# Kernel tuning notes

Hardware: AMD Instinct MI355X
Metric: run time of the kernel (lower is better)

## Reference

```python
import jax, jax.numpy as jnp
import numpy as np

DIM = 1024
EPS_LN = 1e-5
EPS_MEM = 1e-6

def _layernorm(x, g, b):
    mu = jnp.mean(x, axis=-1, keepdims=True)
    var = jnp.mean((x - mu) ** 2, axis=-1, keepdims=True)
    return (x - mu) * jax.lax.rsqrt(var + EPS_LN) * g + b

def setup_inputs() -> dict:
    key = jax.random.key(0)
    ks = jax.random.split(key, 8)
    B, S, D = 4, 4096, DIM
    s1 = 1.0 / np.sqrt(D)
    s2 = 1.0 / np.sqrt(4 * D)
    return {
        "x": jax.random.normal(ks[0], (B, S, D), dtype=jnp.float32),
        "ln1_g": jnp.ones((D,), jnp.float32),
        "ln1_b": jnp.zeros((D,), jnp.float32),
        "ln2_g": jnp.ones((D,), jnp.float32),
        "ln2_b": jnp.zeros((D,), jnp.float32),
        "gate_w": jax.random.uniform(ks[1], (D, D), jnp.float32, -s1, s1),
        "gate_b": jax.random.uniform(ks[2], (D,), jnp.float32, -s1, s1),
        "value_w": jax.random.uniform(ks[3], (D, D), jnp.float32, -s1, s1),
        "value_b": jax.random.uniform(ks[4], (D,), jnp.float32, -s1, s1),
        "ffn_w1": jax.random.uniform(ks[5], (D, 4 * D), jnp.float32, -s1, s1),
        "ffn_b1": jnp.zeros((4 * D,), jnp.float32),
        "ffn_w2": jax.random.uniform(ks[6], (4 * D, D), jnp.float32, -s2, s2),
        "ffn_b2": jnp.zeros((D,), jnp.float32),
    }

def reference(x, ln1_g, ln1_b, ln2_g, ln2_b, gate_w, gate_b, value_w, value_b, ffn_w1, ffn_b1, ffn_w2, ffn_b2):
    h = _layernorm(x, ln1_g, ln1_b)
    g = jax.nn.sigmoid(h @ gate_w + gate_b)
    v = h @ value_w + value_b
    cumsum_v = jnp.cumsum(g * v, axis=1)
    cumsum_g = jnp.cumsum(g, axis=1) + EPS_MEM
    x = x + cumsum_v / cumsum_g
    h2 = _layernorm(x, ln2_g, ln2_b)
    ffn = jax.nn.gelu(h2 @ ffn_w1 + ffn_b1, approximate=False) @ ffn_w2 + ffn_b2
    return x + ffn
```

## Files before the change

### kernel.cpp

```cpp
#include <hip/hip_runtime.h>
#include <cstdint>
#include <cstddef>

#define D_MODEL 1024
#define SEQ     4096
#define BATCH   4
#define M_ROWS  (BATCH*SEQ)
#define NCHUNK  64
#define LCHUNK  (SEQ/NCHUNK)

typedef __bf16 bf16_t;
typedef __bf16 bf16x8 __attribute__((ext_vector_type(8)));
typedef __bf16 bf16x4 __attribute__((ext_vector_type(4)));
typedef float  f32x4  __attribute__((ext_vector_type(4)));

__device__ __forceinline__ void load_lds_128(const bf16_t* g, bf16_t* l) {
    __builtin_amdgcn_global_load_lds(
        (const __attribute__((address_space(1))) unsigned int*)g,
        (__attribute__((address_space(3))) unsigned int*)l,
        16, 0, 0);
}

__device__ __forceinline__ float2 bf16pair_to_f2(unsigned int u) {
    union { unsigned int i; float f; } a, b;
    a.i = u << 16;
    b.i = u & 0xffff0000u;
    float2 r; r.x = a.f; r.y = b.f; return r;
}

__global__ __launch_bounds__(256)
void transpose_all(const float* __restrict__ gate_w, const float* __restrict__ value_w,
                   const float* __restrict__ ffn_w1, const float* __restrict__ ffn_w2,
                   bf16_t* __restrict__ wgv_t, bf16_t* __restrict__ w1_t,
                   bf16_t* __restrict__ w2_t) {
    int id = blockIdx.x;
    const float* in; bf16_t* outp; int R, C, bx, by;
    if (id < 1024)      { in = gate_w;  outp = wgv_t;               R = 1024; C = 1024; bx = id & 31;  by = id >> 5; }
    else if (id < 2048) { id -= 1024; in = value_w; outp = wgv_t + 1024*1024; R = 1024; C = 1024; bx = id & 31;  by = id >> 5; }
    else if (id < 6144) { id -= 2048; in = ffn_w1;  outp = w1_t;    R = 1024; C = 4096; bx = id & 127; by = id >> 7; }
    else                { id -= 6144; in = ffn_w2;  outp = w2_t;    R = 4096; C = 1024; bx = id & 31;  by = id >> 5; }
    __shared__ float t[32][33];
    int tx = threadIdx.x & 31, ty = threadIdx.x >> 5;
    int c0 = bx * 32, r0 = by * 32;
    #pragma unroll
    for (int j = 0; j < 32; j += 8)
        t[ty + j][tx] = in[(size_t)(r0 + ty + j) * C + c0 + tx];
    __syncthreads();
    #pragma unroll
    for (int j = 0; j < 32; j += 8)
        outp[(size_t)(c0 + ty + j) * R + r0 + tx] = (bf16_t)t[tx][ty + j];
}

__global__ __launch_bounds__(256)
void ln_kernel(const float* __restrict__ x, const float* __restrict__ gamma,
               const float* __restrict__ beta, bf16_t* __restrict__ h) {
    int row = blockIdx.x;
    int tid = threadIdx.x;
    const float4* xr = (const float4*)(x + (size_t)row * D_MODEL);
    float4 v = xr[tid];
    float s  = v.x + v.y + v.z + v.w;
    float ss = v.x*v.x + v.y*v.y + v.z*v.z + v.w*v.w;
    #pragma unroll
    for (int off = 32; off; off >>= 1) {
        s  += __shfl_down(s, off);
        ss += __shfl_down(ss, off);
    }
    __shared__ float red[8];
    int wave = tid >> 6, lane = tid & 63;
    if (lane == 0) { red[wave] = s; red[4 + wave] = ss; }
    __syncthreads();
    if (tid == 0) {
        float S  = red[0] + red[1] + red[2] + red[3];
        float SS = red[4] + red[5] + red[6] + red[7];
        float mean = S * (1.0f / D_MODEL);
        float var  = SS * (1.0f / D_MODEL) - mean * mean;
        red[0] = mean;
        red[1] = rsqrtf(var + 1e-5f);
    }
    __syncthreads();
    float mean = red[0], rstd = red[1];
    float4 gv = ((const float4*)gamma)[tid];
    float4 bv = ((const float4*)beta)[tid];
    bf16x4 o;
    o[0] = (bf16_t)((v.x - mean) * rstd * gv.x + bv.x);
    o[1] = (bf16_t)((v.y - mean) * rstd * gv.y + bv.y);
    o[2] = (bf16_t)((v.z - mean) * rstd * gv.z + bv.z);
    o[3] = (bf16_t)((v.w - mean) * rstd * gv.w + bv.w);
    ((bf16x4*)h)[(size_t)row * (D_MODEL / 4) + tid] = o;
}

template <int MODE, int TN>
__global__ __launch_bounds__(256, 4)
void gemm_kernel(const bf16_t* __restrict__ A, const bf16_t* __restrict__ Bt,
                 const float* __restrict__ bias, const float* __restrict__ bias2,
                 const float* __restrict__ xres,
                 void* __restrict__ out, void* __restrict__ out2,
                 int M, int N, int K) {
    __shared__ __align__(16) bf16_t ldsA[128 * 64];
    __shared__ __align__(16) bf16_t ldsB[128 * 64];

    const int tid  = threadIdx.x;
    const int lane = tid & 63;
    const int wave = tid >> 6;
    const int wm   = wave & 1;
    const int wn   = wave >> 1;

    const int L  = blockIdx.x;
    const int r  = L >> 3;
    const int n0 = (r % TN) * 128;
    const int m0 = ((L & 7) + 8 * (r / TN)) * 128;

    f32x4 acc[4][4];
    f32x4 zero = {0.f, 0.f, 0.f, 0.f};
    #pragma unroll
    for (int i = 0; i < 4; i++)
        #pragma unroll
        for (int j = 0; j < 4; j++) acc[i][j] = zero;

    const int rl     = lane >> 3;
    const int srcCol = ((lane & 7) ^ rl) * 8;

    const int quad = lane >> 4;
    const int l16  = lane & 15;
    const int rswz = l16 & 7;

    for (int k0 = 0; k0 < K; k0 += 64) {
        __syncthreads();
        #pragma unroll
        for (int i = 0; i < 4; i++) {
            int cb = i * 4 + wave;
            int rr = cb * 8 + rl;
            load_lds_128(A  + (size_t)(m0 + rr) * K + k0 + srcCol,
                         ldsA + cb * 512 + lane * 8);
            load_lds_128(Bt + (size_t)(n0 + rr) * K + k0 + srcCol,
                         ldsB + cb * 512 + lane * 8);
        }
        __syncthreads();

        #pragma unroll
        for (int kk = 0; kk < 2; kk++) {
            int pos = ((quad + 4 * kk) ^ rswz) * 8;
            bf16x8 af[4], bfr[4];
            #pragma unroll
            for (int mt = 0; mt < 4; mt++)
                af[mt] = *(const bf16x8*)(ldsA + (wm * 64 + mt * 16 + l16) * 64 + pos);
            #pragma unroll
            for (int nt = 0; nt < 4; nt++)
                bfr[nt] = *(const bf16x8*)(ldsB + (wn * 64 + nt * 16 + l16) * 64 + pos);
            #pragma unroll
            for (int mt = 0; mt < 4; mt++)
                #pragma unroll
                for (int nt = 0; nt < 4; nt++)
                    acc[mt][nt] = __builtin_amdgcn_mfma_f32_16x16x32_bf16(
                        bfr[nt], af[mt], acc[mt][nt], 0, 0, 0);
        }
    }

    #pragma unroll
    for (int mt = 0; mt < 4; mt++) {
        int row = m0 + wm * 64 + mt * 16 + l16;
        #pragma unroll
        for (int nt = 0; nt < 4; nt++) {
            int col = n0 + wn * 64 + nt * 16 + quad * 4;
            f32x4 a = acc[mt][nt];
            if (MODE == 4) {
                bool isV = (n0 >= 1024);
                int c1 = col & 1023;
                float4 bv = *(const float4*)((isV ? bias2 : bias) + c1);
                float4 val;
                val.x = a[0] + bv.x; val.y = a[1] + bv.y;
                val.z = a[2] + bv.z; val.w = a[3] + bv.w;
                if (!isV) {
                    val.x = 1.0f / (1.0f + __expf(-val.x));
                    val.y = 1.0f / (1.0f + __expf(-val.y));
                    val.z = 1.0f / (1.0f + __expf(-val.z));
                    val.w = 1.0f / (1.0f + __expf(-val.w));
                }
                bf16x4 p;
                p[0] = (bf16_t)val.x; p[1] = (bf16_t)val.y;
                p[2] = (bf16_t)val.z; p[3] = (bf16_t)val.w;
                bf16_t* o = (bf16_t*)(isV ? out2 : out);
                *(bf16x4*)(o + (size_t)row * 1024 + c1) = p;
            } else if (MODE == 2) {
                float4 bv = *(const float4*)(bias + col);
                float4 val;
                val.x = a[0] + bv.x; val.y = a[1] + bv.y;
                val.z = a[2] + bv.z; val.w = a[3] + bv.w;
                val.x = 0.5f * val.x * (1.0f + erff(val.x * 0.70710678118654752f));
                val.y = 0.5f * val.y * (1.0f + erff(val.y * 0.70710678118654752f));
                val.z = 0.5f * val.z * (1.0f + erff(val.z * 0.70710678118654752f));
                val.w = 0.5f * val.w * (1.0f + erff(val.w * 0.70710678118654752f));
                bf16x4 p;
                p[0] = (bf16_t)val.x; p[1] = (bf16_t)val.y;
                p[2] = (bf16_t)val.z; p[3] = (bf16_t)val.w;
                *(bf16x4*)((bf16_t*)out + (size_t)row * N + col) = p;
            } else {
                float4 bv = *(const float4*)(bias + col);
                float4 xr = *(const float4*)(xres + (size_t)row * N + col);
                float4 val;
                val.x = xr.x + a[0] + bv.x; val.y = xr.y + a[1] + bv.y;
                val.z = xr.z + a[2] + bv.z; val.w = xr.w + a[3] + bv.w;
                *(float4*)((float*)out + (size_t)row * N + col) = val;
            }
        }
    }
}

__global__ __launch_bounds__(256)
void scan_partial(const bf16_t* __restrict__ g, const bf16_t* __restrict__ v,
                  float* __restrict__ sg, float* __restrict__ sgv) {
    int dt = blockIdx.x & 1;
    int c  = (blockIdx.x >> 1) & (NCHUNK - 1);
    int b  = blockIdx.x >> 7;
    int d  = dt * 512 + threadIdx.x * 2;
    float s0 = 0.f, s1 = 0.f, t0 = 0.f, t1 = 0.f;
    for (int i = 0; i < LCHUNK; i++) {
        int s = c * LCHUNK + i;
        size_t idx = ((size_t)(b * SEQ + s)) * D_MODEL + d;
        float2 gf = bf16pair_to_f2(*(const unsigned int*)(g + idx));
        float2 vf = bf16pair_to_f2(*(const unsigned int*)(v + idx));
        s0 += gf.x; s1 += gf.y;
        t0 += gf.x * vf.x; t1 += gf.y * vf.y;
    }
    size_t o = ((size_t)(b * NCHUNK + c)) * D_MODEL + d;
    sg[o] = s0;  sg[o + 1] = s1;
    sgv[o] = t0; sgv[o + 1] = t1;
}

__global__ __launch_bounds__(256)
void scan_apply(const bf16_t* __restrict__ g, const bf16_t* __restrict__ v,
                const float* __restrict__ x, const float* __restrict__ sg,
                const float* __restrict__ sgv, float* __restrict__ out) {
    int dt = blockIdx.x & 1;
    int c  = (blockIdx.x >> 1) & (NCHUNK - 1);
    int b  = blockIdx.x >> 7;
    int d  = dt * 512 + threadIdx.x * 2;
    float rg0 = 0.f, rg1 = 0.f, rv0 = 0.f, rv1 = 0.f;
    for (int p = 0; p < c; p++) {
        size_t o = ((size_t)(b * NCHUNK + p)) * D_MODEL + d;
        float2 a  = *(const float2*)(sg + o);
        float2 bb = *(const float2*)(sgv + o);
        rg0 += a.x;  rg1 += a.y;
        rv0 += bb.x; rv1 += bb.y;
    }
    for (int i = 0; i < LCHUNK; i++) {
        int s = c * LCHUNK + i;
        size_t idx = ((size_t)(b * SEQ + s)) * D_MODEL + d;
        float2 gf = bf16pair_to_f2(*(const unsigned int*)(g + idx));
        float2 vf = bf16pair_to_f2(*(const unsigned int*)(v + idx));
        rv0 += gf.x * vf.x; rg0 += gf.x;
        rv1 += gf.y * vf.y; rg1 += gf.y;
        float2 xv = *(const float2*)(x + idx);
        float2 ov;
        ov.x = xv.x + rv0 / (rg0 + 1e-6f);
        ov.y = xv.y + rv1 / (rg1 + 1e-6f);
        *(float2*)(out + idx) = ov;
    }
}

extern "C" void kernel_launch(void* const* d_in, const int* in_sizes, int n_in,
                              void* d_out, int out_size, void* d_ws, size_t ws_size,
                              hipStream_t stream) {
    (void)in_sizes; (void)n_in; (void)out_size; (void)ws_size;
    const float* x       = (const float*)d_in[0];
    const float* ln1_g   = (const float*)d_in[1];
    const float* ln1_b   = (const float*)d_in[2];
    const float* ln2_g   = (const float*)d_in[3];
    const float* ln2_b   = (const float*)d_in[4];
    const float* gate_w  = (const float*)d_in[5];
    const float* gate_b  = (const float*)d_in[6];
    const float* value_w = (const float*)d_in[7];
    const float* value_b = (const float*)d_in[8];
    const float* ffn_w1  = (const float*)d_in[9];
    const float* ffn_b1  = (const float*)d_in[10];
    const float* ffn_w2  = (const float*)d_in[11];
    const float* ffn_b2  = (const float*)d_in[12];
    float* out = (float*)d_out;

    char* ws = (char*)d_ws;
    const size_t MB = 1024 * 1024;
    bf16_t* wgv_t = (bf16_t*)(ws + 0 * MB);
    bf16_t* w1_t  = (bf16_t*)(ws + 4 * MB);
    bf16_t* w2_t  = (bf16_t*)(ws + 12 * MB);
    bf16_t* h     = (bf16_t*)(ws + 20 * MB);
    bf16_t* g     = (bf16_t*)(ws + 52 * MB);
    bf16_t* v     = (bf16_t*)(ws + 84 * MB);
    float*  sg    = (float*)(ws + 116 * MB);
    float*  sgv   = (float*)(ws + 117 * MB);
    bf16_t* act   = (bf16_t*)(ws + 118 * MB);

    transpose_all<<<10240, 256, 0, stream>>>(gate_w, value_w, ffn_w1, ffn_w2,
                                             wgv_t, w1_t, w2_t);

    ln_kernel<<<M_ROWS, 256, 0, stream>>>(x, ln1_g, ln1_b, h);

    gemm_kernel<4, 16><<<(2048 / 128) * (M_ROWS / 128), 256, 0, stream>>>(
        h, wgv_t, gate_b, value_b, nullptr, g, v, M_ROWS, 2048, 1024);

    scan_partial<<<BATCH * NCHUNK * 2, 256, 0, stream>>>(g, v, sg, sgv);
    scan_apply<<<BATCH * NCHUNK * 2, 256, 0, stream>>>(g, v, x, sg, sgv, out);

    ln_kernel<<<M_ROWS, 256, 0, stream>>>(out, ln2_g, ln2_b, h);

    gemm_kernel<2, 32><<<(4096 / 128) * (M_ROWS / 128), 256, 0, stream>>>(
        h, w1_t, ffn_b1, nullptr, nullptr, act, nullptr, M_ROWS, 4096, 1024);

    gemm_kernel<3, 8><<<(1024 / 128) * (M_ROWS / 128), 256, 0, stream>>>(
        act, w2_t, ffn_b2, nullptr, out, out, nullptr, M_ROWS, 1024, 4096);
}
```

Measured before the change: 637.3 us.

## Replace GEMM with 256x256 double-buffered 8-wave pipelined kernel

Replaces the 128x128 single-buffered GEMM with a 256x256 tile kernel using 512 threads, double-buffered LDS, and a phased schedule. The schedule interleaves global-to-LDS loads with MFMA groups, using barriers and s_setprio. The aim is to overlap memory traffic with compute and to raise reuse per loaded tile. In exchange it uses 128 KB of LDS and many accumulator registers per block, which limits occupancy to one block per CU and risks register pressure. All three GEMM launches are updated with the new grid sizes.

```diff
diff --git a/kernel.cpp b/kernel.cpp
--- a/kernel.cpp
+++ b/kernel.cpp
@@ -89,78 +89,126 @@
     ((bf16x4*)h)[(size_t)row * (D_MODEL / 4) + tid] = o;
 }
 
+#define PHASE_MID() do { __builtin_amdgcn_s_barrier(); \
+    asm volatile("s_waitcnt lgkmcnt(0)" ::: "memory"); \
+    __builtin_amdgcn_s_setprio(1); } while (0)
+#define PHASE_END() do { __builtin_amdgcn_s_setprio(0); \
+    __builtin_amdgcn_s_barrier(); } while (0)
+#define PHASE_END_VM() do { __builtin_amdgcn_s_setprio(0); \
+    asm volatile("s_waitcnt vmcnt(4)" ::: "memory"); \
+    __builtin_amdgcn_s_barrier(); } while (0)
+
+#define LDA4(BUF, MB) do { _Pragma("unroll") for (int m_ = 0; m_ < 4; ++m_) { \
+    af[m_][0] = *(const bf16x8*)((BUF) + aoff0 + ((MB)*4 + m_) * 1024); \
+    af[m_][1] = *(const bf16x8*)((BUF) + aoff1 + ((MB)*4 + m_) * 1024); } } while (0)
+#define LDB2(BUF, NLO) do { _Pragma("unroll") for (int n_ = 0; n_ < 2; ++n_) { \
+    bfr[(NLO)+n_][0] = *(const bf16x8*)((BUF) + boff0 + ((NLO)+n_) * 1024); \
+    bfr[(NLO)+n_][1] = *(const bf16x8*)((BUF) + boff1 + ((NLO)+n_) * 1024); } } while (0)
+#define MFMA_HALF(MB, NLO) do { _Pragma("unroll") for (int m_ = 0; m_ < 4; ++m_) { \
+    _Pragma("unroll") for (int n_ = 0; n_ < 2; ++n_) { \
+        acc[(MB)*4 + m_][(NLO) + n_] = __builtin_amdgcn_mfma_f32_16x16x32_bf16( \
+            bfr[(NLO)+n_][0], af[m_][0], acc[(MB)*4 + m_][(NLO) + n_], 0, 0, 0); \
+        acc[(MB)*4 + m_][(NLO) + n_] = __builtin_amdgcn_mfma_f32_16x16x32_bf16( \
+            bfr[(NLO)+n_][1], af[m_][1], acc[(MB)*4 + m_][(NLO) + n_], 0, 0, 0); } } } while (0)
+
 template <int MODE, int TN>
-__global__ __launch_bounds__(256, 4)
-void gemm_kernel(const bf16_t* __restrict__ A, const bf16_t* __restrict__ Bt,
-                 const float* __restrict__ bias, const float* __restrict__ bias2,
-                 const float* __restrict__ xres,
-                 void* __restrict__ out, void* __restrict__ out2,
-                 int M, int N, int K) {
-    __shared__ __align__(16) bf16_t ldsA[128 * 64];
-    __shared__ __align__(16) bf16_t ldsB[128 * 64];
+__global__ __launch_bounds__(512, 2)
+void gemm256(const bf16_t* __restrict__ A, const bf16_t* __restrict__ Bt,
+             const float* __restrict__ bias, const float* __restrict__ bias2,
+             const float* __restrict__ xres,
+             void* __restrict__ out, void* __restrict__ out2,
+             int M, int N, int K) {
+    __shared__ __align__(16) bf16_t lds[2][2][256 * 64];
 
     const int tid  = threadIdx.x;
     const int lane = tid & 63;
     const int wave = tid >> 6;
-    const int wm   = wave & 1;
-    const int wn   = wave >> 1;
+    const int wm   = wave >> 2;
+    const int wn   = wave & 3;
 
     const int L  = blockIdx.x;
     const int r  = L >> 3;
-    const int n0 = (r % TN) * 128;
-    const int m0 = ((L & 7) + 8 * (r / TN)) * 128;
-
-    f32x4 acc[4][4];
-    f32x4 zero = {0.f, 0.f, 0.f, 0.f};
-    #pragma unroll
-    for (int i = 0; i < 4; i++)
+    const int n0 = (r % TN) * 256;
+    const int m0 = ((L & 7) + 8 * (r / TN)) * 256;
+
+    f32x4 acc[8][4];
+    #pragma unroll
+    for (int i = 0; i < 8; i++)
         #pragma unroll
-        for (int j = 0; j < 4; j++) acc[i][j] = zero;
-
-    const int rl     = lane >> 3;
-    const int srcCol = ((lane & 7) ^ rl) * 8;
-
-    const int quad = lane >> 4;
-    const int l16  = lane & 15;
-    const int rswz = l16 & 7;
-
-    for (int k0 = 0; k0 < K; k0 += 64) {
-        __syncthreads();
+        for (int j = 0; j < 4; j++) acc[i][j] = (f32x4){0.f, 0.f, 0.f, 0.f};
+
+    const int rr = tid >> 3;
+    const int sc = ((tid & 7) ^ (rr & 7)) * 8;
+    const bf16_t* pa = A  + ((size_t)(m0 + rr)) * K + sc;
+    const bf16_t* pb = Bt + ((size_t)(n0 + rr)) * K + sc;
+    const size_t rstep = (size_t)64 * K;
+    const size_t hstep = rstep * 2;
+
+    const int l16 = lane & 15, quad = lane >> 4, swz = l16 & 7;
+    const int aoff0 = (wm*128 + l16)*64 + ((quad    ) ^ swz)*8;
+    const int aoff1 = (wm*128 + l16)*64 + ((quad + 4) ^ swz)*8;
+    const int boff0 = (wn*64  + l16)*64 + ((quad    ) ^ swz)*8;
+    const int boff1 = (wn*64  + l16)*64 + ((quad + 4) ^ swz)*8;
+
+    bf16_t* LA0 = &lds[0][0][0]; bf16_t* LB0 = &lds[0][1][0];
+    bf16_t* LA1 = &lds[1][0][0]; bf16_t* LB1 = &lds[1][1][0];
+
+    const int KT = K >> 6;
+    const int NI = KT >> 1;
+
+    auto STAGE = [&](const bf16_t* gsrc, bf16_t* dst) {
+        load_lds_128(gsrc,         dst + tid * 8);
+        load_lds_128(gsrc + rstep, dst + 4096 + tid * 8);
+    };
+
+    STAGE(pb,              LB0);
+    STAGE(pb + hstep,      LB0 + 8192);
+    STAGE(pa,              LA0);
+    STAGE(pa + hstep,      LA0 + 8192);
+    STAGE(pb + 64,         LB1);
+    STAGE(pb + hstep + 64, LB1 + 8192);
+    asm volatile("s_waitcnt vmcnt(4)" ::: "memory");
+    __builtin_amdgcn_s_barrier();
+
+    for (int it = 0; it < NI; ++it) {
+        const int k1 = (2*it + 1) * 64;
+        const int t2 = (2*it + 2 < KT) ? 2*it + 2 : KT - 1;
+        const int t3 = (2*it + 3 < KT) ? 2*it + 3 : KT - 1;
+        const int k2 = t2 * 64, k3 = t3 * 64;
+
+        bf16x8 af[4][2], bfr[4][2];
+
+        LDA4(LA0, 0); LDB2(LB0, 0);
+        STAGE(pa + k1, LA1);
+        PHASE_MID(); MFMA_HALF(0, 0); PHASE_END();
+        LDB2(LB0, 2);
+        STAGE(pa + hstep + k1, LA1 + 8192);
+        PHASE_MID(); MFMA_HALF(0, 2); PHASE_END();
+        LDA4(LA0, 1);
+        STAGE(pb + k2, LB0);
+        PHASE_MID(); MFMA_HALF(1, 0); PHASE_END();
+        STAGE(pb + hstep + k2, LB0 + 8192);
+        PHASE_MID(); MFMA_HALF(1, 2); PHASE_END_VM();
+        LDA4(LA1, 0); LDB2(LB1, 0);
+        STAGE(pa + k2, LA0);
+        PHASE_MID(); MFMA_HALF(0, 0); PHASE_END();
+        LDB2(LB1, 2);
+        STAGE(pa + hstep + k2, LA0 + 8192);
+        PHASE_MID(); MFMA_HALF(0, 2); PHASE_END();
+        LDA4(LA1, 1);
+        STAGE(pb + k3, LB1);
+        PHASE_MID(); MFMA_HALF(1, 0); PHASE_END();
+        STAGE(pb + hstep + k3, LB1 + 8192);
+        PHASE_MID(); MFMA_HALF(1, 2); PHASE_END_VM();
+    }
+
+    asm volatile("s_waitcnt vmcnt(0)" ::: "memory");
+
+    #pragma unroll
+    for (int mt = 0; mt < 8; ++mt) {
+        int row = m0 + wm * 128 + mt * 16 + l16;
         #pragma unroll
-        for (int i = 0; i < 4; i++) {
-            int cb = i * 4 + wave;
-            int rr = cb * 8 + rl;
-            load_lds_128(A  + (size_t)(m0 + rr) * K + k0 + srcCol,
-                         ldsA + cb * 512 + lane * 8);
-            load_lds_128(Bt + (size_t)(n0 + rr) * K + k0 + srcCol,
-                         ldsB + cb * 512 + lane * 8);
-        }
-        __syncthreads();
-
-        #pragma unroll
-        for (int kk = 0; kk < 2; kk++) {
-            int pos = ((quad + 4 * kk) ^ rswz) * 8;
-            bf16x8 af[4], bfr[4];
-            #pragma unroll
-            for (int mt = 0; mt < 4; mt++)
-                af[mt] = *(const bf16x8*)(ldsA + (wm * 64 + mt * 16 + l16) * 64 + pos);
-            #pragma unroll
-            for (int nt = 0; nt < 4; nt++)
-                bfr[nt] = *(const bf16x8*)(ldsB + (wn * 64 + nt * 16 + l16) * 64 + pos);
-            #pragma unroll
-            for (int mt = 0; mt < 4; mt++)
-                #pragma unroll
-                for (int nt = 0; nt < 4; nt++)
-                    acc[mt][nt] = __builtin_amdgcn_mfma_f32_16x16x32_bf16(
-                        bfr[nt], af[mt], acc[mt][nt], 0, 0, 0);
-        }
-    }
-
-    #pragma unroll
-    for (int mt = 0; mt < 4; mt++) {
-        int row = m0 + wm * 64 + mt * 16 + l16;
-        #pragma unroll
-        for (int nt = 0; nt < 4; nt++) {
+        for (int nt = 0; nt < 4; ++nt) {
             int col = n0 + wn * 64 + nt * 16 + quad * 4;
             f32x4 a = acc[mt][nt];
             if (MODE == 4) {
@@ -294,7 +342,7 @@
 
     ln_kernel<<<M_ROWS, 256, 0, stream>>>(x, ln1_g, ln1_b, h);
 
-    gemm_kernel<4, 16><<<(2048 / 128) * (M_ROWS / 128), 256, 0, stream>>>(
+    gemm256<4, 8><<<8 * 64, 512, 0, stream>>>(
         h, wgv_t, gate_b, value_b, nullptr, g, v, M_ROWS, 2048, 1024);
 
     scan_partial<<<BATCH * NCHUNK * 2, 256, 0, stream>>>(g, v, sg, sgv);
@@ -302,9 +350,9 @@
 
     ln_kernel<<<M_ROWS, 256, 0, stream>>>(out, ln2_g, ln2_b, h);
 
-    gemm_kernel<2, 32><<<(4096 / 128) * (M_ROWS / 128), 256, 0, stream>>>(
+    gemm256<2, 16><<<16 * 64, 512, 0, stream>>>(
         h, w1_t, ffn_b1, nullptr, nullptr, act, nullptr, M_ROWS, 4096, 1024);
 
-    gemm_kernel<3, 8><<<(1024 / 128) * (M_ROWS / 128), 256, 0, stream>>>(
+    gemm256<3, 4><<<4 * 64, 512, 0, stream>>>(
         act, w2_t, ffn_b2, nullptr, out, out, nullptr, M_ROWS, 1024, 4096);
 }
```

Measured after the change: 621.1 us. 1.03x faster.
